# Performance work log

Measured on AMD Instinct MI355X. Metric: run time of the kernel, lower is better.

The kernel has to match this reference:

```python
import jax, jax.numpy as jnp
import numpy as np

B, NPOS, NNEG, D, NLEM = 8, 512, 512, 128, 32768
MOMENTUM = 0.5
EPS = 1e-12  # F.normalize eps


def setup_inputs() -> dict:
    key = jax.random.key(0)
    k1, k2, k3, k4 = jax.random.split(key, 4)
    x = jax.random.normal(k1, (B, NPOS + NNEG, D), dtype=jnp.float32)
    y = jax.random.randint(k2, (B, NPOS), 0, NPOS).astype(jnp.int64)
    visible = jax.random.randint(k3, (B, NPOS), 0, 2).astype(jnp.int32)
    stdv = 1.0 / np.sqrt(D / 3.0)
    memory = jax.random.uniform(k4, (NLEM, D), dtype=jnp.float32,
                                minval=-stdv, maxval=stdv)
    return {"x": x, "y": y, "visible": visible, "memory": memory, "lru": 3}


def reference(x, y, visible, memory, lru):
    # --- similarity computation (differentiable path) ---
    t = x[:, :NPOS, :]                                  # [B, NPOS, D]
    similarity = jnp.einsum('bpd,md->bpm', t, memory)    # [B, NPOS, NLEM]
    noise_similarity = jnp.einsum('bnd,pd->bnp',
                                  x[:, NPOS:, :], memory[:NPOS])  # [B, NNEG, NPOS]
    y_idx = y.astype(jnp.int64)

    # --- memory bank update (no-grad in original) ---
    vis = visible.astype(x.dtype)[..., None]             # [B, NPOS, 1]
    get = jnp.mean(t * vis, axis=0)                      # [NPOS, D]
    pos_new = memory[:NPOS] * MOMENTUM + get * (1.0 - MOMENTUM)
    neg_flat = x[:, NPOS:, :].reshape(-1, D)             # [B*NNEG, D]
    start = NPOS + lru * NNEG * B                        # lru is a python int
    new_mem = memory.at[start:start + NNEG * B].set(neg_flat)
    new_mem = new_mem.at[:NPOS].set(pos_new)
    norms = jnp.maximum(jnp.linalg.norm(new_mem, axis=1, keepdims=True), EPS)
    new_mem = jax.lax.stop_gradient(new_mem / norms)

    return similarity, y_idx, noise_similarity, new_mem
```

## Files before the change

### kernel.cpp

```cpp
#include <hip/hip_runtime.h>
#include <hip/hip_bf16.h>
#include <cstdint>

#define NPOS 512
#define NNEG 512
#define BATCH 8
#define DDIM 128
#define NLEM 32768
#define NX_ELEM (BATCH * (NPOS + NNEG) * DDIM)
#define NM_ELEM (NLEM * DDIM)
#define GRID_GEMM 256
#define NT_TILES 8320

typedef __attribute__((ext_vector_type(4))) float f32x4;
typedef __attribute__((ext_vector_type(16))) float f32x16;
typedef __attribute__((ext_vector_type(8))) short short8;

__device__ __forceinline__ unsigned short f2bf(float f) {
  unsigned u = __float_as_uint(f);
  u = (u + 0x7FFFu + ((u >> 16) & 1u)) >> 16;
  return (unsigned short)u;
}

__device__ __forceinline__ short8 cvt8(f32x4 a0, f32x4 a1) {
  short8 w;
  w[0] = (short)f2bf(a0[0]); w[1] = (short)f2bf(a0[1]);
  w[2] = (short)f2bf(a0[2]); w[3] = (short)f2bf(a0[3]);
  w[4] = (short)f2bf(a1[0]); w[5] = (short)f2bf(a1[1]);
  w[6] = (short)f2bf(a1[2]); w[7] = (short)f2bf(a1[3]);
  return w;
}

__device__ __forceinline__ void async16(const void* g, void* l) {
  __builtin_amdgcn_global_load_lds(
      (const __attribute__((address_space(1))) unsigned int*)g,
      (__attribute__((address_space(3))) unsigned int*)l, 16, 0, 0);
}

__device__ __forceinline__ void newmem_row(int r, int lane, const float* __restrict__ X,
                                           const int* __restrict__ vis,
                                           const float* __restrict__ Mem, int start,
                                           float* __restrict__ out) {
  const int d0 = lane, d1 = lane + 64;
  float v0, v1;
  if (r < NPOS) {
    const float s0 = Mem[(size_t)r * DDIM + d0];
    const float s1 = Mem[(size_t)r * DDIM + d1];
    float a0 = 0.f, a1 = 0.f;
#pragma unroll
    for (int b = 0; b < BATCH; ++b) {
      const float w = (float)vis[b * NPOS + r];
      const float* px = X + (size_t)(b * (NPOS + NNEG) + r) * DDIM;
      a0 += w * px[d0];
      a1 += w * px[d1];
    }
    v0 = 0.5f * s0 + 0.0625f * a0;
    v1 = 0.5f * s1 + 0.0625f * a1;
  } else if (r >= start && r < start + BATCH * NNEG) {
    const int q = r - start;
    const int b = q >> 9, n = q & 511;
    const float* px = X + (size_t)(b * (NPOS + NNEG) + NPOS + n) * DDIM;
    v0 = px[d0];
    v1 = px[d1];
  } else {
    v0 = Mem[(size_t)r * DDIM + d0];
    v1 = Mem[(size_t)r * DDIM + d1];
  }
  float s = v0 * v0 + v1 * v1;
#pragma unroll
  for (int off = 32; off; off >>= 1) s += __shfl_xor(s, off, 64);
  const float inv = 1.0f / fmaxf(sqrtf(s), 1e-12f);
  out[(size_t)r * DDIM + d0] = v0 * inv;
  out[(size_t)r * DDIM + d1] = v1 * inv;
}

__global__ __launch_bounds__(256) void prep_kernel(
    const float* __restrict__ X, const int* __restrict__ y,
    const int* __restrict__ vis, const float* __restrict__ Mem,
    const int* __restrict__ lru_p, unsigned short* __restrict__ xb,
    unsigned short* __restrict__ mb, float* __restrict__ out_y,
    float* __restrict__ out_mem) {
  const int blk = blockIdx.x;
  if (blk < 512) {
    const size_t i = ((size_t)blk * 256 + threadIdx.x) * 8;
    *(short8*)(xb + i) = cvt8(*(const f32x4*)(X + i), *(const f32x4*)(X + i + 4));
  } else if (blk < 2560) {
    const size_t i = ((size_t)(blk - 512) * 256 + threadIdx.x) * 8;
    *(short8*)(mb + i) = cvt8(*(const f32x4*)(Mem + i), *(const f32x4*)(Mem + i + 4));
  } else if (blk < 2576) {
    const int i = (blk - 2560) * 256 + threadIdx.x;
    out_y[i] = (float)y[i];
  } else {
    const int r = (blk - 2576) * 4 + (threadIdx.x >> 6);
    const int start = NPOS + lru_p[0] * (NNEG * BATCH);
    newmem_row(r, threadIdx.x & 63, X, vis, Mem, start, out_mem);
  }
}

__global__ __launch_bounds__(256) void gemm_persist_kernel(
    const unsigned short* __restrict__ Xb, const unsigned short* __restrict__ Mb,
    float* __restrict__ Csim, float* __restrict__ Cnoise) {
  __shared__ short lds[2][2][128 * 128];

  const int t = threadIdx.x;
  const int lane = t & 63, wv = t >> 6;
  const int rl = lane >> 4, slot = lane & 15;
  const int wr = wv >> 1, wc = wv & 1;
  const int la = lane & 31, lb = lane >> 5;

  const int b = blockIdx.x;
  const int nk = (NT_TILES - b + GRID_GEMM - 1) / GRID_GEMM;

  auto stage = [&](int p, int T) {
    const int m0 = (T & 31) * 128;
    const int by = T >> 5;
    const int n0 = (by < 256 ? by : by - 256) * 128;
    const int a_off = (by < 256) ? 0 : NPOS;
    const int xbase = ((m0 >> 9) << 10) + (m0 & 511) + a_off;
    short* A = lds[p][0];
    short* B = lds[p][1];
#pragma unroll
    for (int i = 0; i < 8; ++i) {
      const int rowb = wv * 32 + i * 4;
      const int row = rowb + rl;
      const int ss = slot ^ (row & 15);
      async16(Xb + (size_t)(xbase + row) * DDIM + ss * 8, &A[rowb * 128]);
      async16(Mb + (size_t)(n0 + row) * DDIM + ss * 8, &B[rowb * 128]);
    }
  };

  stage(0, b);
  asm volatile("s_waitcnt vmcnt(0)" ::: "memory");
  __builtin_amdgcn_s_barrier();
  __builtin_amdgcn_sched_barrier(0);

  int p = 0;
  for (int k = 0; k < nk; ++k) {
    const int T = b + k * GRID_GEMM;
    if (k + 1 < nk) stage(p ^ 1, T + GRID_GEMM);

    const short* A = lds[p][0];
    const short* B = lds[p][1];
    f32x16 acc[2][2] = {};
#pragma unroll
    for (int kk = 0; kk < 8; ++kk) {
      short8 af[2], bfr[2];
#pragma unroll
      for (int m2 = 0; m2 < 2; ++m2) {
        const int row = wr * 64 + m2 * 32 + la;
        const int ss = ((kk * 2 + lb) ^ (row & 15)) * 8;
        af[m2] = *(const short8*)&A[row * 128 + ss];
      }
#pragma unroll
      for (int n2 = 0; n2 < 2; ++n2) {
        const int row = wc * 64 + n2 * 32 + la;
        const int ss = ((kk * 2 + lb) ^ (row & 15)) * 8;
        bfr[n2] = *(const short8*)&B[row * 128 + ss];
      }
#pragma unroll
      for (int m2 = 0; m2 < 2; ++m2)
#pragma unroll
        for (int n2 = 0; n2 < 2; ++n2)
          acc[m2][n2] = __builtin_amdgcn_mfma_f32_32x32x16_bf16(
              af[m2], bfr[n2], acc[m2][n2], 0, 0, 0);
    }

    const int m0 = (T & 31) * 128;
    const int by = T >> 5;
    float* C;
    int ldc, n0c;
    if (by < 256) { C = Csim; ldc = NLEM; n0c = by * 128; }
    else          { C = Cnoise; ldc = NPOS; n0c = (by - 256) * 128; }
#pragma unroll
    for (int m2 = 0; m2 < 2; ++m2) {
#pragma unroll
      for (int n2 = 0; n2 < 2; ++n2) {
        const int col = n0c + wc * 64 + n2 * 32 + la;
        const int rbase = m0 + wr * 64 + m2 * 32 + lb * 4;
#pragma unroll
        for (int r = 0; r < 16; ++r) {
          const int row = rbase + (r & 3) + 8 * (r >> 2);
          C[(size_t)row * ldc + col] = acc[m2][n2][r];
        }
      }
    }

    if (k + 1 < nk) {
      asm volatile("s_waitcnt vmcnt(60)" ::: "memory");
      __builtin_amdgcn_s_barrier();
      __builtin_amdgcn_sched_barrier(0);
    }
    p ^= 1;
  }
}

__global__ __launch_bounds__(256) void gemm_conv_kernel(
    const float* __restrict__ X, const float* __restrict__ Bm,
    float* __restrict__ C, int ldc, int a_off) {
  __shared__ short lds[2 * 128 * 128];
  short* ldsA = lds;
  short* ldsB = lds + 128 * 128;
  const int t = threadIdx.x;
  const int m0 = blockIdx.x * 128;
  const int n0 = blockIdx.y * 128;
  const int slot = t & 15;
  const int rsub = t >> 4;
#pragma unroll
  for (int it = 0; it < 8; ++it) {
    const int row = it * 16 + rsub;
    const int gr = m0 + row;
    const int xrow = ((gr >> 9) << 10) + (gr & 511) + a_off;
    const f32x4* pa = (const f32x4*)(X + (size_t)xrow * DDIM + slot * 8);
    const f32x4* pb = (const f32x4*)(Bm + (size_t)(n0 + row) * DDIM + slot * 8);
    short8 wa = cvt8(pa[0], pa[1]);
    short8 wb = cvt8(pb[0], pb[1]);
    const int ss = (slot ^ (row & 15)) * 8;
    *(short8*)&ldsA[row * 128 + ss] = wa;
    *(short8*)&ldsB[row * 128 + ss] = wb;
  }
  __syncthreads();
  const int lane = t & 63;
  const int wv = t >> 6;
  const int wr = wv >> 1, wc = wv & 1;
  const int la = lane & 31, lb = lane >> 5;
  f32x16 acc[2][2] = {};
#pragma unroll
  for (int kk = 0; kk < 8; ++kk) {
    short8 af[2], bfr[2];
#pragma unroll
    for (int m2 = 0; m2 < 2; ++m2) {
      const int row = wr * 64 + m2 * 32 + la;
      const int ss = ((kk * 2 + lb) ^ (row & 15)) * 8;
      af[m2] = *(const short8*)&ldsA[row * 128 + ss];
    }
#pragma unroll
    for (int n2 = 0; n2 < 2; ++n2) {
      const int row = wc * 64 + n2 * 32 + la;
      const int ss = ((kk * 2 + lb) ^ (row & 15)) * 8;
      bfr[n2] = *(const short8*)&ldsB[row * 128 + ss];
    }
#pragma unroll
    for (int m2 = 0; m2 < 2; ++m2)
#pragma unroll
      for (int n2 = 0; n2 < 2; ++n2)
        acc[m2][n2] = __builtin_amdgcn_mfma_f32_32x32x16_bf16(
            af[m2], bfr[n2], acc[m2][n2], 0, 0, 0);
  }
#pragma unroll
  for (int m2 = 0; m2 < 2; ++m2)
#pragma unroll
    for (int n2 = 0; n2 < 2; ++n2) {
      const int col = n0 + wc * 64 + n2 * 32 + la;
      const int rbase = m0 + wr * 64 + m2 * 32 + lb * 4;
#pragma unroll
      for (int r = 0; r < 16; ++r) {
        const int row = rbase + (r & 3) + 8 * (r >> 2);
        C[(size_t)row * ldc + col] = acc[m2][n2][r];
      }
    }
}

__global__ void y_kernel(const int* __restrict__ y, float* __restrict__ out) {
  const int i = blockIdx.x * blockDim.x + threadIdx.x;
  if (i < BATCH * NPOS) out[i] = (float)y[i];
}

__global__ __launch_bounds__(256) void newmem_kernel(
    const float* __restrict__ X, const int* __restrict__ vis,
    const float* __restrict__ Mem, const int* __restrict__ lru_p,
    float* __restrict__ out) {
  const int r = blockIdx.x * 4 + (threadIdx.x >> 6);
  const int start = NPOS + lru_p[0] * (NNEG * BATCH);
  newmem_row(r, threadIdx.x & 63, X, vis, Mem, start, out);
}

extern "C" void kernel_launch(void* const* d_in, const int* in_sizes, int n_in,
                              void* d_out, int out_size, void* d_ws, size_t ws_size,
                              hipStream_t stream) {
  const float* x = (const float*)d_in[0];
  const int* y = (const int*)d_in[1];
  const int* visible = (const int*)d_in[2];
  const float* memory = (const float*)d_in[3];
  const int* lru = (const int*)d_in[4];
  float* out = (float*)d_out;

  const size_t OFF_Y = (size_t)BATCH * NPOS * NLEM;
  const size_t OFF_NOISE = OFF_Y + (size_t)BATCH * NPOS;
  const size_t OFF_MEM = OFF_NOISE + (size_t)BATCH * NNEG * NPOS;

  const size_t need = (size_t)(NX_ELEM + NM_ELEM) * 2;
  if (ws_size >= need) {
    unsigned short* xb = (unsigned short*)d_ws;
    unsigned short* mb = xb + NX_ELEM;
    prep_kernel<<<2576 + NLEM / 4, 256, 0, stream>>>(
        x, y, visible, memory, lru, xb, mb, out + OFF_Y, out + OFF_MEM);
    gemm_persist_kernel<<<GRID_GEMM, 256, 0, stream>>>(
        xb, mb, out, out + OFF_NOISE);
  } else {
    gemm_conv_kernel<<<dim3(32, 256), 256, 0, stream>>>(x, memory, out, NLEM, 0);
    gemm_conv_kernel<<<dim3(32, 4), 256, 0, stream>>>(x, memory, out + OFF_NOISE, NPOS, NPOS);
    y_kernel<<<16, 256, 0, stream>>>(y, out + OFF_Y);
    newmem_kernel<<<NLEM / 4, 256, 0, stream>>>(x, visible, memory, lru, out + OFF_MEM);
  }
}
```

Before: 132.1 us.

## Hold memory tile in registers per block and stream X band tiles

The persistent GEMM is replaced by a band kernel where each of 256 blocks owns one 128-column slice of memory, loads its B fragments into registers once, and streams the 32 positive-row tiles of X through double-buffered LDS. The noise GEMM moves to a separate fp32 conversion GEMM launch, and prep only converts the positive half of X to bf16. This removes repeated B tile loads and LDS reads per tile and halves the X conversion work, at the cost of higher register pressure (launch bounds of 1) and an extra kernel launch.

```diff
diff --git a/kernel.cpp b/kernel.cpp
--- a/kernel.cpp
+++ b/kernel.cpp
@@ -9,8 +9,7 @@
 #define NLEM 32768
 #define NX_ELEM (BATCH * (NPOS + NNEG) * DDIM)
 #define NM_ELEM (NLEM * DDIM)
-#define GRID_GEMM 256
-#define NT_TILES 8320
+#define NK_STEPS 32
 
 typedef __attribute__((ext_vector_type(4))) float f32x4;
 typedef __attribute__((ext_vector_type(16))) float f32x16;
@@ -81,111 +80,109 @@
     unsigned short* __restrict__ mb, float* __restrict__ out_y,
     float* __restrict__ out_mem) {
   const int blk = blockIdx.x;
-  if (blk < 512) {
-    const size_t i = ((size_t)blk * 256 + threadIdx.x) * 8;
+  if (blk < 256) {
+    const size_t i = (size_t)(blk >> 5) * 131072 + (size_t)(blk & 31) * 2048 +
+                     (size_t)threadIdx.x * 8;
     *(short8*)(xb + i) = cvt8(*(const f32x4*)(X + i), *(const f32x4*)(X + i + 4));
-  } else if (blk < 2560) {
-    const size_t i = ((size_t)(blk - 512) * 256 + threadIdx.x) * 8;
+  } else if (blk < 2304) {
+    const size_t i = ((size_t)(blk - 256) * 256 + threadIdx.x) * 8;
     *(short8*)(mb + i) = cvt8(*(const f32x4*)(Mem + i), *(const f32x4*)(Mem + i + 4));
-  } else if (blk < 2576) {
-    const int i = (blk - 2560) * 256 + threadIdx.x;
+  } else if (blk < 2320) {
+    const int i = (blk - 2304) * 256 + threadIdx.x;
     out_y[i] = (float)y[i];
   } else {
-    const int r = (blk - 2576) * 4 + (threadIdx.x >> 6);
+    const int r = (blk - 2320) * 4 + (threadIdx.x >> 6);
     const int start = NPOS + lru_p[0] * (NNEG * BATCH);
     newmem_row(r, threadIdx.x & 63, X, vis, Mem, start, out_mem);
   }
 }
 
-__global__ __launch_bounds__(256) void gemm_persist_kernel(
+__global__ __launch_bounds__(256, 1) void gemm_band_kernel(
     const unsigned short* __restrict__ Xb, const unsigned short* __restrict__ Mb,
-    float* __restrict__ Csim, float* __restrict__ Cnoise) {
-  __shared__ short lds[2][2][128 * 128];
+    float* __restrict__ Csim) {
+  __shared__ short ldsA[2][128 * 128];
+  __shared__ short ldsB[128 * 128];
 
   const int t = threadIdx.x;
   const int lane = t & 63, wv = t >> 6;
   const int rl = lane >> 4, slot = lane & 15;
   const int wr = wv >> 1, wc = wv & 1;
   const int la = lane & 31, lb = lane >> 5;
-
   const int b = blockIdx.x;
-  const int nk = (NT_TILES - b + GRID_GEMM - 1) / GRID_GEMM;
-
-  auto stage = [&](int p, int T) {
-    const int m0 = (T & 31) * 128;
-    const int by = T >> 5;
-    const int n0 = (by < 256 ? by : by - 256) * 128;
-    const int a_off = (by < 256) ? 0 : NPOS;
-    const int xbase = ((m0 >> 9) << 10) + (m0 & 511) + a_off;
-    short* A = lds[p][0];
-    short* B = lds[p][1];
+  const int n0 = b * 128;
+
+  auto stageA = [&](int p, int k) {
+    const int m0 = k * 128;
+    const int xbase = ((m0 >> 9) << 10) + (m0 & 511);
 #pragma unroll
     for (int i = 0; i < 8; ++i) {
       const int rowb = wv * 32 + i * 4;
       const int row = rowb + rl;
       const int ss = slot ^ (row & 15);
-      async16(Xb + (size_t)(xbase + row) * DDIM + ss * 8, &A[rowb * 128]);
-      async16(Mb + (size_t)(n0 + row) * DDIM + ss * 8, &B[rowb * 128]);
+      async16(Xb + (size_t)(xbase + row) * DDIM + ss * 8, &ldsA[p][rowb * 128]);
     }
   };
 
-  stage(0, b);
+#pragma unroll
+  for (int i = 0; i < 8; ++i) {
+    const int rowb = wv * 32 + i * 4;
+    const int row = rowb + rl;
+    const int ss = slot ^ (row & 15);
+    async16(Mb + (size_t)(n0 + row) * DDIM + ss * 8, &ldsB[rowb * 128]);
+  }
+  stageA(0, 0);
   asm volatile("s_waitcnt vmcnt(0)" ::: "memory");
   __builtin_amdgcn_s_barrier();
   __builtin_amdgcn_sched_barrier(0);
 
+  short8 bfr[8][2];
+#pragma unroll
+  for (int kk = 0; kk < 8; ++kk)
+#pragma unroll
+    for (int n2 = 0; n2 < 2; ++n2) {
+      const int row = wc * 64 + n2 * 32 + la;
+      const int ss = ((kk * 2 + lb) ^ (row & 15)) * 8;
+      bfr[kk][n2] = *(const short8*)&ldsB[row * 128 + ss];
+    }
+
   int p = 0;
-  for (int k = 0; k < nk; ++k) {
-    const int T = b + k * GRID_GEMM;
-    if (k + 1 < nk) stage(p ^ 1, T + GRID_GEMM);
-
-    const short* A = lds[p][0];
-    const short* B = lds[p][1];
+  for (int k = 0; k < NK_STEPS; ++k) {
+    if (k + 1 < NK_STEPS) stageA(p ^ 1, k + 1);
+
     f32x16 acc[2][2] = {};
 #pragma unroll
     for (int kk = 0; kk < 8; ++kk) {
-      short8 af[2], bfr[2];
+      short8 af[2];
 #pragma unroll
       for (int m2 = 0; m2 < 2; ++m2) {
         const int row = wr * 64 + m2 * 32 + la;
         const int ss = ((kk * 2 + lb) ^ (row & 15)) * 8;
-        af[m2] = *(const short8*)&A[row * 128 + ss];
-      }
-#pragma unroll
-      for (int n2 = 0; n2 < 2; ++n2) {
-        const int row = wc * 64 + n2 * 32 + la;
-        const int ss = ((kk * 2 + lb) ^ (row & 15)) * 8;
-        bfr[n2] = *(const short8*)&B[row * 128 + ss];
+        af[m2] = *(const short8*)&ldsA[p][row * 128 + ss];
       }
 #pragma unroll
       for (int m2 = 0; m2 < 2; ++m2)
 #pragma unroll
         for (int n2 = 0; n2 < 2; ++n2)
           acc[m2][n2] = __builtin_amdgcn_mfma_f32_32x32x16_bf16(
-              af[m2], bfr[n2], acc[m2][n2], 0, 0, 0);
-    }
-
-    const int m0 = (T & 31) * 128;
-    const int by = T >> 5;
-    float* C;
-    int ldc, n0c;
-    if (by < 256) { C = Csim; ldc = NLEM; n0c = by * 128; }
-    else          { C = Cnoise; ldc = NPOS; n0c = (by - 256) * 128; }
+              af[m2], bfr[kk][n2], acc[m2][n2], 0, 0, 0);
+    }
+
+    const int m0 = k * 128;
 #pragma unroll
     for (int m2 = 0; m2 < 2; ++m2) {
 #pragma unroll
       for (int n2 = 0; n2 < 2; ++n2) {
-        const int col = n0c + wc * 64 + n2 * 32 + la;
+        const int col = n0 + wc * 64 + n2 * 32 + la;
         const int rbase = m0 + wr * 64 + m2 * 32 + lb * 4;
 #pragma unroll
         for (int r = 0; r < 16; ++r) {
           const int row = rbase + (r & 3) + 8 * (r >> 2);
-          C[(size_t)row * ldc + col] = acc[m2][n2][r];
+          Csim[(size_t)row * NLEM + col] = acc[m2][n2][r];
         }
       }
     }
 
-    if (k + 1 < nk) {
+    if (k + 1 < NK_STEPS) {
       asm volatile("s_waitcnt vmcnt(60)" ::: "memory");
       __builtin_amdgcn_s_barrier();
       __builtin_amdgcn_sched_barrier(0);
@@ -292,10 +289,10 @@
   if (ws_size >= need) {
     unsigned short* xb = (unsigned short*)d_ws;
     unsigned short* mb = xb + NX_ELEM;
-    prep_kernel<<<2576 + NLEM / 4, 256, 0, stream>>>(
+    gemm_conv_kernel<<<dim3(32, 4), 256, 0, stream>>>(x, memory, out + OFF_NOISE, NPOS, NPOS);
+    prep_kernel<<<10512, 256, 0, stream>>>(
         x, y, visible, memory, lru, xb, mb, out + OFF_Y, out + OFF_MEM);
-    gemm_persist_kernel<<<GRID_GEMM, 256, 0, stream>>>(
-        xb, mb, out, out + OFF_NOISE);
+    gemm_band_kernel<<<256, 256, 0, stream>>>(xb, mb, out);
   } else {
     gemm_conv_kernel<<<dim3(32, 256), 256, 0, stream>>>(x, memory, out, NLEM, 0);
     gemm_conv_kernel<<<dim3(32, 4), 256, 0, stream>>>(x, memory, out + OFF_NOISE, NPOS, NPOS);
```

Measured after the change: 125.7 us. 4.8% less time.
